# Kernel tuning notes

Hardware: AMD Instinct MI355X
Metric: run time of the kernel (lower is better)

The kernel has to match this reference:

```python
import jax, jax.numpy as jnp
import numpy as np

N_NODES = 20000
N_EDGES = 320000
IN_DIM = 512
HID = 256
N_GRAPHS = 256


def setup_inputs() -> dict:
    key = jax.random.key(0)
    ks = jax.random.split(key, 7)
    x = jax.random.normal(ks[0], (N_NODES, IN_DIM), dtype=jnp.float32)
    edge_index = jax.random.randint(ks[1], (2, N_EDGES), 0, N_NODES, dtype=jnp.int64)
    batch = jnp.sort(jax.random.randint(ks[2], (N_NODES,), 0, N_GRAPHS, dtype=jnp.int64))
    W = jax.random.normal(ks[3], (IN_DIM, HID), dtype=jnp.float32) * (1.0 / np.sqrt(IN_DIM))
    b = jax.random.normal(ks[4], (HID,), dtype=jnp.float32) * 0.02
    lin_w = jax.random.normal(ks[5], (HID, 1), dtype=jnp.float32) * (1.0 / np.sqrt(HID))
    lin_b = jax.random.normal(ks[6], (1,), dtype=jnp.float32) * 0.02
    return {"x": x, "edge_index": edge_index, "batch": batch,
            "W": W, "b": b, "lin_w": lin_w, "lin_b": lin_b}


def reference(x, edge_index, batch, W, b, lin_w, lin_b):
    N = x.shape[0]
    # --- GCNConv: add self-loops, symmetric normalization ---
    loop = jnp.arange(N, dtype=edge_index.dtype)
    src = jnp.concatenate([edge_index[0], loop])   # [E+N]
    dst = jnp.concatenate([edge_index[1], loop])   # [E+N]
    deg = jax.ops.segment_sum(jnp.ones_like(dst, dtype=x.dtype), dst, num_segments=N)
    dinv = jnp.where(deg > 0, jax.lax.rsqrt(deg), 0.0)          # [N]
    norm = dinv[src] * dinv[dst]                                 # [E+N]
    h = x @ W                                                    # [N, HID] dense GEMM
    msgs = h[src] * norm[:, None]                                # gather + scale
    agg = jax.ops.segment_sum(msgs, dst, num_segments=N) + b     # scatter-add
    xr = jax.nn.relu(agg)                                        # [N, HID]
    # --- global_mean_pool over graph ids ---
    sums = jax.ops.segment_sum(xr, batch, num_segments=N_GRAPHS)             # [G, HID]
    counts = jax.ops.segment_sum(jnp.ones((N,), dtype=x.dtype), batch, num_segments=N_GRAPHS)
    pooled = sums / jnp.maximum(counts, 1.0)[:, None]
    # --- linear head + sigmoid ---
    out = jax.nn.sigmoid(pooled @ lin_w + lin_b)                 # [G, 1]
    return out.reshape(-1)
```

## Files before the change

kernel.cpp:

```cpp
#include <hip/hip_runtime.h>
#include <hip/hip_bf16.h>
#include <cstdint>

typedef __attribute__((ext_vector_type(8))) _Float16 half8;
typedef __attribute__((ext_vector_type(4))) _Float16 half4;
typedef __attribute__((ext_vector_type(2))) float f32x2;
typedef __attribute__((ext_vector_type(4))) float f32x4;

#define N_NODES 20000
#define N_EDGES 320000
#define IN_DIM 512
#define HID 256
#define N_GRAPHS 256
#define NPB 8
#define DSTRIDE 64

#define PREP_WBLK 16
#define PREP_ZBLK ((N_NODES + 255) / 256)
#define ZTHREADS  (PREP_ZBLK * 256)
__global__ __launch_bounds__(256) void prep_kernel(const float* __restrict__ W,
                                                   _Float16* __restrict__ wt,
                                                   int* __restrict__ cnt2,
                                                   float* __restrict__ sums,
                                                   int* __restrict__ counts) {
    int b = blockIdx.x, t = threadIdx.x;
    if (b < PREP_WBLK) {
        __shared__ _Float16 tile[32 * 256];
        int k0 = b * 32;
        const float4* wp = reinterpret_cast<const float4*>(W + (size_t)k0 * HID);
#pragma unroll
        for (int i = 0; i < 8; ++i) {
            float4 v = wp[i * 256 + t];
            int flat = (i * 256 + t) * 4;
            int kk = flat >> 8, n = flat & 255;
            half4 hv;
            hv[0] = (_Float16)v.x; hv[1] = (_Float16)v.y;
            hv[2] = (_Float16)v.z; hv[3] = (_Float16)v.w;
            *reinterpret_cast<half4*>(&tile[kk * 256 + n]) = hv;
        }
        __syncthreads();
        alignas(16) _Float16 vals[32];
#pragma unroll
        for (int kk = 0; kk < 32; ++kk) vals[kk] = tile[kk * 256 + t];
        uint4* op = reinterpret_cast<uint4*>((char*)wt + (size_t)t * 1024 + (size_t)k0 * 2);
        const uint4* vp = reinterpret_cast<const uint4*>(vals);
#pragma unroll
        for (int j = 0; j < 4; ++j) op[j] = vp[j];
    } else {
        int id = (b - PREP_WBLK) * 256 + t;
        if (id < N_NODES) cnt2[id] = 0;
        if (id < N_GRAPHS) counts[id] = 0;
        for (int j = id; j < N_GRAPHS * HID; j += ZTHREADS) sums[j] = 0.f;
    }
}

#define GEMM_BLOCKS ((N_NODES + 63) / 64)
#define CSR_BLOCKS  (N_EDGES / 256)

#define LOADA(Sa, Sb, Sc, Sd, k0) do { const float* ap_ = aptr + (k0); \
    Sa = *reinterpret_cast<const float4*>(ap_);         \
    Sb = *reinterpret_cast<const float4*>(ap_ + 4);     \
    Sc = *reinterpret_cast<const float4*>(ap_ + 32);    \
    Sd = *reinterpret_cast<const float4*>(ap_ + 36); } while (0)

#define PACKA(Sa, Sb, Sc, Sd) do { \
    a0[0]=(_Float16)Sa.x; a0[1]=(_Float16)Sa.y; a0[2]=(_Float16)Sa.z; a0[3]=(_Float16)Sa.w; \
    a0[4]=(_Float16)Sb.x; a0[5]=(_Float16)Sb.y; a0[6]=(_Float16)Sb.z; a0[7]=(_Float16)Sb.w; \
    a1[0]=(_Float16)Sc.x; a1[1]=(_Float16)Sc.y; a1[2]=(_Float16)Sc.z; a1[3]=(_Float16)Sc.w; \
    a1[4]=(_Float16)Sd.x; a1[5]=(_Float16)Sd.y; a1[6]=(_Float16)Sd.z; a1[7]=(_Float16)Sd.w; } while (0)

#define LOADB(s) do { const uint4* ws_ = wsrc + 8 * (s); \
    wb0=ws_[0]; wb1=ws_[1]; wb2=ws_[2]; wb3=ws_[3];      \
    wb4=ws_[4]; wb5=ws_[5]; wb6=ws_[6]; wb7=ws_[7]; } while (0)

#define STAGEB(q) do { uint4* d_ = reinterpret_cast<uint4*>(myst + ((q) << 15)); \
    d_[0^tsw]=wb0; d_[1^tsw]=wb1; d_[2^tsw]=wb2; d_[3^tsw]=wb3;                  \
    d_[4^tsw]=wb4; d_[5^tsw]=wb5; d_[6^tsw]=wb6; d_[7^tsw]=wb7; } while (0)

#define KBARRIER() do { asm volatile("s_waitcnt lgkmcnt(0)" ::: "memory"); \
    __builtin_amdgcn_s_barrier(); asm volatile("" ::: "memory"); } while (0)

#define MFMASTEP(q) do { const char* rb_ = (const char*)bsl + ((q) << 15); \
    _Pragma("unroll")                                                      \
    for (int nt = 0; nt < 16; ++nt) {                                      \
        int c_ = nt * 16 + col; int cs_ = c_ & 7;                          \
        half8 bb0_ = *reinterpret_cast<const half8*>(rb_ + c_ * 128 + ((quad ^ cs_) << 4));       \
        acc[nt] = __builtin_amdgcn_mfma_f32_16x16x32_f16(a0, bb0_, acc[nt], 0, 0, 0);             \
        half8 bb1_ = *reinterpret_cast<const half8*>(rb_ + c_ * 128 + (((4 + quad) ^ cs_) << 4)); \
        acc[nt] = __builtin_amdgcn_mfma_f32_16x16x32_f16(a1, bb1_, acc[nt], 0, 0, 0);             \
    } } while (0)

__global__ __launch_bounds__(256, 2) void gemm_csr_kernel(const float* __restrict__ x,
                                                          const _Float16* __restrict__ wt,
                                                          unsigned char* __restrict__ h8,
                                                          const int* __restrict__ src,
                                                          const int* __restrict__ dst,
                                                          int* __restrict__ cnt2,
                                                          int* __restrict__ csr) {
    __shared__ _Float16 bsl[2 * 256 * 64];
    if (blockIdx.x >= GEMM_BLOCKS) {
        int e = (blockIdx.x - GEMM_BLOCKS) * 256 + threadIdx.x;
        int d = dst[e];
        int slot = atomicAdd(&cnt2[d], 1);
        if (slot < DSTRIDE) csr[d * DSTRIDE + slot] = src[e];
        return;
    }
    const int K = IN_DIM;
    int t    = threadIdx.x;
    int lane = t & 63;
    int wave = t >> 6;
    int col  = lane & 15;
    int quad = lane >> 4;
    int row0 = blockIdx.x * 64 + wave * 16;

    f32x4 acc[16];
#pragma unroll
    for (int i = 0; i < 16; ++i) acc[i] = (f32x4){0.f, 0.f, 0.f, 0.f};

    int arow = row0 + col;
    if (arow >= N_NODES) arow = N_NODES - 1;
    const float* aptr = x + (size_t)arow * K + quad * 8;
    const uint4* wsrc = reinterpret_cast<const uint4*>(wt + (size_t)t * K);

    char* myst = (char*)bsl + t * 128;
    int tsw = t & 7;

    float4 sA0, sA1, sA2, sA3;
    float4 sB0, sB1, sB2, sB3;
    uint4  wb0, wb1, wb2, wb3, wb4, wb5, wb6, wb7;
    half8  a0, a1;

    LOADB(0);
    LOADA(sA0, sA1, sA2, sA3, 0);
    LOADA(sB0, sB1, sB2, sB3, 64);
    STAGEB(0);
    LOADB(1);
    KBARRIER();

#pragma unroll
    for (int it = 0; it < 4; ++it) {
        PACKA(sA0, sA1, sA2, sA3);
        if (it < 3) LOADA(sA0, sA1, sA2, sA3, (2 * it + 2) * 64);
        STAGEB(1);
        if (it < 3) LOADB(2 * it + 2);
        MFMASTEP(0);
        KBARRIER();
        PACKA(sB0, sB1, sB2, sB3);
        if (it < 3) LOADA(sB0, sB1, sB2, sB3, (2 * it + 3) * 64);
        if (it < 3) { STAGEB(0); LOADB(2 * it + 3); }
        MFMASTEP(1);
        KBARRIER();
    }

    int orow0 = row0 + quad * 4;
#pragma unroll
    for (int nt = 0; nt < 16; ++nt) {
#pragma unroll
        for (int r = 0; r < 4; ++r) {
            int rr = orow0 + r;
            if (rr < N_NODES) {
                float v = acc[nt][r];
                int pk = __builtin_amdgcn_cvt_pk_fp8_f32(v, v, 0, false);
                h8[(size_t)rr * HID + nt * 16 + col] = (unsigned char)(pk & 0xff);
            }
        }
    }
}

#define AGG_BLOCKS  (N_NODES / NPB)
#define HIST_BLOCKS ((N_NODES + 255) / 256)
__global__ __launch_bounds__(256, 8) void aggregate_kernel(const unsigned char* __restrict__ h8,
                                                           const float* __restrict__ bias,
                                                           const int* __restrict__ cnt2,
                                                           const int* __restrict__ csr,
                                                           const int* __restrict__ batch,
                                                           float* __restrict__ sums,
                                                           int* __restrict__ counts) {
    if (blockIdx.x >= AGG_BLOCKS) {
        int id = (blockIdx.x - AGG_BLOCKS) * 256 + threadIdx.x;
        if (id < N_NODES) atomicAdd(&counts[batch[id]], 1);
        return;
    }
    __shared__ float pool[NPB * HID];
    int v0  = blockIdx.x * NPB;
    int t   = threadIdx.x;
    int grp = t >> 6;
    int fl  = t & 63;
    int vg  = v0 + grp * 2;
    const float4 bf = *reinterpret_cast<const float4*>(bias + 4 * fl);

    float a0[2], a1[2], a2[2], a3[2], dvv[2];
#pragma unroll
    for (int i = 0; i < 2; ++i) {
        int v = vg + i;
        int ctrue = cnt2[v];
        int cnt = ctrue; if (cnt > DSTRIDE) cnt = DSTRIDE;
        float dv = rsqrtf((float)ctrue + 1.f);
        dvv[i] = dv;
        unsigned int u = *reinterpret_cast<const unsigned int*>(h8 + (size_t)v * HID + 4 * fl);
        f32x2 lo = __builtin_amdgcn_cvt_pk_f32_fp8(u, false);
        f32x2 hi = __builtin_amdgcn_cvt_pk_f32_fp8(u, true);
        float x0 = dv * lo[0], x1 = dv * lo[1], x2 = dv * hi[0], x3 = dv * hi[1];
        int ecv = csr[v * DSTRIDE + fl];
        int j = 0;
        for (; j + 4 <= cnt; j += 4) {
            int s0 = __shfl(ecv, j, 64);
            int s1 = __shfl(ecv, j + 1, 64);
            int s2 = __shfl(ecv, j + 2, 64);
            int s3 = __shfl(ecv, j + 3, 64);
            int c0 = cnt2[s0], c1 = cnt2[s1], c2 = cnt2[s2], c3 = cnt2[s3];
            unsigned int u0 = *reinterpret_cast<const unsigned int*>(h8 + (size_t)s0 * HID + 4 * fl);
            unsigned int u1 = *reinterpret_cast<const unsigned int*>(h8 + (size_t)s1 * HID + 4 * fl);
            unsigned int u2 = *reinterpret_cast<const unsigned int*>(h8 + (size_t)s2 * HID + 4 * fl);
            unsigned int u3 = *reinterpret_cast<const unsigned int*>(h8 + (size_t)s3 * HID + 4 * fl);
            float d0 = rsqrtf((float)c0 + 1.f);
            float d1 = rsqrtf((float)c1 + 1.f);
            float d2 = rsqrtf((float)c2 + 1.f);
            float d3 = rsqrtf((float)c3 + 1.f);
            f32x2 p;
            p = __builtin_amdgcn_cvt_pk_f32_fp8(u0, false); x0 += d0 * p[0]; x1 += d0 * p[1];
            p = __builtin_amdgcn_cvt_pk_f32_fp8(u0, true);  x2 += d0 * p[0]; x3 += d0 * p[1];
            p = __builtin_amdgcn_cvt_pk_f32_fp8(u1, false); x0 += d1 * p[0]; x1 += d1 * p[1];
            p = __builtin_amdgcn_cvt_pk_f32_fp8(u1, true);  x2 += d1 * p[0]; x3 += d1 * p[1];
            p = __builtin_amdgcn_cvt_pk_f32_fp8(u2, false); x0 += d2 * p[0]; x1 += d2 * p[1];
            p = __builtin_amdgcn_cvt_pk_f32_fp8(u2, true);  x2 += d2 * p[0]; x3 += d2 * p[1];
            p = __builtin_amdgcn_cvt_pk_f32_fp8(u3, false); x0 += d3 * p[0]; x1 += d3 * p[1];
            p = __builtin_amdgcn_cvt_pk_f32_fp8(u3, true);  x2 += d3 * p[0]; x3 += d3 * p[1];
        }
        for (; j < cnt; ++j) {
            int s = __shfl(ecv, j, 64);
            int c = cnt2[s];
            unsigned int u4 = *reinterpret_cast<const unsigned int*>(h8 + (size_t)s * HID + 4 * fl);
            float ds = rsqrtf((float)c + 1.f);
            f32x2 p;
            p = __builtin_amdgcn_cvt_pk_f32_fp8(u4, false); x0 += ds * p[0]; x1 += ds * p[1];
            p = __builtin_amdgcn_cvt_pk_f32_fp8(u4, true);  x2 += ds * p[0]; x3 += ds * p[1];
        }
        a0[i] = x0; a1[i] = x1; a2[i] = x2; a3[i] = x3;
    }

#pragma unroll
    for (int i = 0; i < 2; ++i) {
        f32x4 r;
        r[0] = fmaxf(dvv[i] * a0[i] + bf.x, 0.f);
        r[1] = fmaxf(dvv[i] * a1[i] + bf.y, 0.f);
        r[2] = fmaxf(dvv[i] * a2[i] + bf.z, 0.f);
        r[3] = fmaxf(dvv[i] * a3[i] + bf.w, 0.f);
        *reinterpret_cast<f32x4*>(&pool[(grp * 2 + i) * HID + 4 * fl]) = r;
    }
    __syncthreads();

    float acc = 0.f;
    int cur_g = batch[v0];
#pragma unroll
    for (int i = 0; i < NPB; ++i) {
        float val = pool[i * HID + t];
        int g = batch[v0 + i];
        if (g != cur_g) {
            atomicAdd(&sums[(size_t)cur_g * HID + t], acc);
            acc = 0.f;
            cur_g = g;
        }
        acc += val;
    }
    atomicAdd(&sums[(size_t)cur_g * HID + t], acc);
}

__global__ __launch_bounds__(256) void head_kernel(const float* __restrict__ sums,
                                                   const int* __restrict__ counts,
                                                   const float* __restrict__ lin_w,
                                                   const float* __restrict__ lin_b,
                                                   float* __restrict__ out) {
    int g = blockIdx.x;
    int f = threadIdx.x;
    float c = (float)counts[g];
    if (c < 1.f) c = 1.f;
    float v = (sums[(size_t)g * HID + f] / c) * lin_w[f];
#pragma unroll
    for (int off = 32; off >= 1; off >>= 1) v += __shfl_down(v, off, 64);
    __shared__ float red[4];
    if ((f & 63) == 0) red[f >> 6] = v;
    __syncthreads();
    if (f == 0) {
        float s = red[0] + red[1] + red[2] + red[3] + lin_b[0];
        out[g] = 1.0f / (1.0f + expf(-s));
    }
}

extern "C" void kernel_launch(void* const* d_in, const int* in_sizes, int n_in,
                              void* d_out, int out_size, void* d_ws, size_t ws_size,
                              hipStream_t stream) {
    const float* x     = (const float*)d_in[0];
    const int*   edge  = (const int*)d_in[1];
    const int*   batch = (const int*)d_in[2];
    const float* W     = (const float*)d_in[3];
    const float* b     = (const float*)d_in[4];
    const float* lin_w = (const float*)d_in[5];
    const float* lin_b = (const float*)d_in[6];
    float*       out   = (float*)d_out;

    const int N = N_NODES, E = N_EDGES, G = N_GRAPHS, K = IN_DIM, H = HID;
    const int* src = edge;
    const int* dst = edge + E;

    char* p = (char*)d_ws;
    auto alloc = [&](size_t bytes) {
        char* r = p;
        p += (bytes + 255) & ~(size_t)255;
        return r;
    };
    _Float16*      wt  = (_Float16*)alloc((size_t)H * K * 2);
    unsigned char* h8  = (unsigned char*)alloc((size_t)N * H);
    int*           csr = (int*)alloc((size_t)N * DSTRIDE * 4);
    int*   cnt2   = (int*)alloc((size_t)N * 4);
    float* sums   = (float*)alloc((size_t)G * H * 4);
    int*   counts = (int*)alloc((size_t)G * 4);

    prep_kernel<<<PREP_WBLK + PREP_ZBLK, 256, 0, stream>>>(W, wt, cnt2, sums, counts);
    gemm_csr_kernel<<<GEMM_BLOCKS + CSR_BLOCKS, 256, 0, stream>>>(x, wt, h8, src, dst,
                                                                  cnt2, csr);
    aggregate_kernel<<<AGG_BLOCKS + HIST_BLOCKS, 256, 0, stream>>>(h8, b, cnt2, csr,
                                                                   batch, sums, counts);
    head_kernel<<<G, 256, 0, stream>>>(sums, counts, lin_w, lin_b, out);
}
```

Measured before the change: 158.6 us.

## Store CSR indices as u16, use nontemporal stores, unroll edge loop by eight

The CSR neighbour indices shrink from int32 to uint16, since node ids fit under 65536, which halves CSR write and read traffic. The CSR and fp8 h8 writes in the GEMM kernel become nontemporal stores. The aggregation gather loop is unrolled to eight edges per iteration so more independent loads are in flight. Nontemporal stores may hurt if h8 would otherwise stay cached for the next kernel, and the wider unroll raises register pressure.

```diff
diff --git a/kernel.cpp b/kernel.cpp
--- a/kernel.cpp
+++ b/kernel.cpp
@@ -96,13 +96,14 @@
                                                           const int* __restrict__ src,
                                                           const int* __restrict__ dst,
                                                           int* __restrict__ cnt2,
-                                                          int* __restrict__ csr) {
+                                                          unsigned short* __restrict__ csr) {
     __shared__ _Float16 bsl[2 * 256 * 64];
     if (blockIdx.x >= GEMM_BLOCKS) {
         int e = (blockIdx.x - GEMM_BLOCKS) * 256 + threadIdx.x;
         int d = dst[e];
         int slot = atomicAdd(&cnt2[d], 1);
-        if (slot < DSTRIDE) csr[d * DSTRIDE + slot] = src[e];
+        if (slot < DSTRIDE)
+            __builtin_nontemporal_store((unsigned short)src[e], &csr[d * DSTRIDE + slot]);
         return;
     }
     const int K = IN_DIM;
@@ -161,7 +162,8 @@
             if (rr < N_NODES) {
                 float v = acc[nt][r];
                 int pk = __builtin_amdgcn_cvt_pk_fp8_f32(v, v, 0, false);
-                h8[(size_t)rr * HID + nt * 16 + col] = (unsigned char)(pk & 0xff);
+                __builtin_nontemporal_store((unsigned char)(pk & 0xff),
+                                            &h8[(size_t)rr * HID + nt * 16 + col]);
             }
         }
     }
@@ -169,10 +171,19 @@
 
 #define AGG_BLOCKS  (N_NODES / NPB)
 #define HIST_BLOCKS ((N_NODES + 255) / 256)
+
+#define EDGE_TERM(SS) do { \
+    int c_ = cnt2[SS]; \
+    unsigned int u_ = *reinterpret_cast<const unsigned int*>(h8 + (size_t)(SS) * HID + 4 * fl); \
+    float d_ = rsqrtf((float)c_ + 1.f); \
+    f32x2 p_; \
+    p_ = __builtin_amdgcn_cvt_pk_f32_fp8(u_, false); x0 += d_ * p_[0]; x1 += d_ * p_[1]; \
+    p_ = __builtin_amdgcn_cvt_pk_f32_fp8(u_, true);  x2 += d_ * p_[0]; x3 += d_ * p_[1]; } while (0)
+
 __global__ __launch_bounds__(256, 8) void aggregate_kernel(const unsigned char* __restrict__ h8,
                                                            const float* __restrict__ bias,
                                                            const int* __restrict__ cnt2,
-                                                           const int* __restrict__ csr,
+                                                           const unsigned short* __restrict__ csr,
                                                            const int* __restrict__ batch,
                                                            float* __restrict__ sums,
                                                            int* __restrict__ counts) {
@@ -201,40 +212,30 @@
         f32x2 lo = __builtin_amdgcn_cvt_pk_f32_fp8(u, false);
         f32x2 hi = __builtin_amdgcn_cvt_pk_f32_fp8(u, true);
         float x0 = dv * lo[0], x1 = dv * lo[1], x2 = dv * hi[0], x3 = dv * hi[1];
-        int ecv = csr[v * DSTRIDE + fl];
+        int ecv = (int)csr[v * DSTRIDE + fl];
         int j = 0;
-        for (; j + 4 <= cnt; j += 4) {
-            int s0 = __shfl(ecv, j, 64);
+        for (; j + 8 <= cnt; j += 8) {
+            int s0 = __shfl(ecv, j,     64);
             int s1 = __shfl(ecv, j + 1, 64);
             int s2 = __shfl(ecv, j + 2, 64);
             int s3 = __shfl(ecv, j + 3, 64);
-            int c0 = cnt2[s0], c1 = cnt2[s1], c2 = cnt2[s2], c3 = cnt2[s3];
-            unsigned int u0 = *reinterpret_cast<const unsigned int*>(h8 + (size_t)s0 * HID + 4 * fl);
-            unsigned int u1 = *reinterpret_cast<const unsigned int*>(h8 + (size_t)s1 * HID + 4 * fl);
-            unsigned int u2 = *reinterpret_cast<const unsigned int*>(h8 + (size_t)s2 * HID + 4 * fl);
-            unsigned int u3 = *reinterpret_cast<const unsigned int*>(h8 + (size_t)s3 * HID + 4 * fl);
-            float d0 = rsqrtf((float)c0 + 1.f);
-            float d1 = rsqrtf((float)c1 + 1.f);
-            float d2 = rsqrtf((float)c2 + 1.f);
-            float d3 = rsqrtf((float)c3 + 1.f);
-            f32x2 p;
-            p = __builtin_amdgcn_cvt_pk_f32_fp8(u0, false); x0 += d0 * p[0]; x1 += d0 * p[1];
-            p = __builtin_amdgcn_cvt_pk_f32_fp8(u0, true);  x2 += d0 * p[0]; x3 += d0 * p[1];
-            p = __builtin_amdgcn_cvt_pk_f32_fp8(u1, false); x0 += d1 * p[0]; x1 += d1 * p[1];
-            p = __builtin_amdgcn_cvt_pk_f32_fp8(u1, true);  x2 += d1 * p[0]; x3 += d1 * p[1];
-            p = __builtin_amdgcn_cvt_pk_f32_fp8(u2, false); x0 += d2 * p[0]; x1 += d2 * p[1];
-            p = __builtin_amdgcn_cvt_pk_f32_fp8(u2, true);  x2 += d2 * p[0]; x3 += d2 * p[1];
-            p = __builtin_amdgcn_cvt_pk_f32_fp8(u3, false); x0 += d3 * p[0]; x1 += d3 * p[1];
-            p = __builtin_amdgcn_cvt_pk_f32_fp8(u3, true);  x2 += d3 * p[0]; x3 += d3 * p[1];
+            int s4 = __shfl(ecv, j + 4, 64);
+            int s5 = __shfl(ecv, j + 5, 64);
+            int s6 = __shfl(ecv, j + 6, 64);
+            int s7 = __shfl(ecv, j + 7, 64);
+            EDGE_TERM(s0); EDGE_TERM(s1); EDGE_TERM(s2); EDGE_TERM(s3);
+            EDGE_TERM(s4); EDGE_TERM(s5); EDGE_TERM(s6); EDGE_TERM(s7);
+        }
+        for (; j + 4 <= cnt; j += 4) {
+            int s0 = __shfl(ecv, j,     64);
+            int s1 = __shfl(ecv, j + 1, 64);
+            int s2 = __shfl(ecv, j + 2, 64);
+            int s3 = __shfl(ecv, j + 3, 64);
+            EDGE_TERM(s0); EDGE_TERM(s1); EDGE_TERM(s2); EDGE_TERM(s3);
         }
         for (; j < cnt; ++j) {
             int s = __shfl(ecv, j, 64);
-            int c = cnt2[s];
-            unsigned int u4 = *reinterpret_cast<const unsigned int*>(h8 + (size_t)s * HID + 4 * fl);
-            float ds = rsqrtf((float)c + 1.f);
-            f32x2 p;
-            p = __builtin_amdgcn_cvt_pk_f32_fp8(u4, false); x0 += ds * p[0]; x1 += ds * p[1];
-            p = __builtin_amdgcn_cvt_pk_f32_fp8(u4, true);  x2 += ds * p[0]; x3 += ds * p[1];
+            EDGE_TERM(s);
         }
         a0[i] = x0; a1[i] = x1; a2[i] = x2; a3[i] = x3;
     }
@@ -309,9 +310,9 @@
         p += (bytes + 255) & ~(size_t)255;
         return r;
     };
-    _Float16*      wt  = (_Float16*)alloc((size_t)H * K * 2);
-    unsigned char* h8  = (unsigned char*)alloc((size_t)N * H);
-    int*           csr = (int*)alloc((size_t)N * DSTRIDE * 4);
+    _Float16*       wt  = (_Float16*)alloc((size_t)H * K * 2);
+    unsigned char*  h8  = (unsigned char*)alloc((size_t)N * H);
+    unsigned short* csr = (unsigned short*)alloc((size_t)N * DSTRIDE * 2);
     int*   cnt2   = (int*)alloc((size_t)N * 4);
     float* sums   = (float*)alloc((size_t)G * H * 4);
     int*   counts = (int*)alloc((size_t)G * 4);
```

Result: slower. 175.8 us (+10.8%).
